# Optimization experiments

Measured on AMD Instinct MI355X. Metric: run time of the kernel, lower is better.

## Reference

```python
import jax, jax.numpy as jnp
import numpy as np

B, L, D, K = 1024, 50, 128, 20
NI, NL, NT = 100000, 10000, 2000  # items, locs, times


def _emb(k, n, d):
    e = jax.random.normal(k, (n, d), dtype=jnp.float32) * 0.02
    return e.at[0].set(0.0)  # padding_idx=0


def setup_inputs() -> dict:
    key = jax.random.key(0)
    ks = jax.random.split(key, 40)
    inp = {}
    inp['item'] = jax.random.randint(ks[0], (B, L), 0, NI)
    inp['locs'] = jax.random.randint(ks[1], (B,), 0, NL)
    inp['times'] = jax.random.randint(ks[2], (B,), 0, NT)
    inp['session_emb'] = jax.random.normal(ks[3], (B, 1, D), dtype=jnp.float32)
    # embedding tables
    inp['loc_emb'] = _emb(ks[4], NL, D)
    inp['time_emb'] = _emb(ks[5], NT, D)
    inp['item_emb'] = _emb(ks[6], NI, D)
    # sampled fixed-fanout neighbor tables Hg[edge]['neighbor']
    inp['nb_IL'] = jax.random.randint(ks[7], (NL, K), 0, NI)   # item neighbors of locs
    inp['nb_TL'] = jax.random.randint(ks[8], (NL, K), 0, NT)   # time neighbors of locs
    inp['nb_IT'] = jax.random.randint(ks[9], (NT, K), 0, NI)   # item neighbors of times
    inp['nb_LT'] = jax.random.randint(ks[10], (NT, K), 0, NL)  # loc neighbors of times
    inp['nb_II'] = jax.random.randint(ks[11], (NI, K), 0, NI)  # item neighbors of items
    inp['nb_LI'] = jax.random.randint(ks[12], (NI, K), 0, NL)  # loc neighbors of items
    inp['nb_TI'] = jax.random.randint(ks[13], (NI, K), 0, NT)  # time neighbors of items
    # 7 HeteAggregator params: Linear(2D -> D) + ReLU
    s = 1.0 / np.sqrt(2 * D)
    names = ['IL', 'TL', 'IT', 'LT', 'II', 'LI', 'TI']
    for i, nm in enumerate(names):
        inp['W_' + nm] = jax.random.uniform(ks[14 + i], (2 * D, D), jnp.float32, -s, s)
        inp['b_' + nm] = jnp.zeros((D,), jnp.float32)
    # 3 SemanticAttention params: Linear(D->D,bias)+tanh, Linear(D->1,no bias)
    s2 = 1.0 / np.sqrt(D)
    for i, nm in enumerate(['l', 't', 'i']):
        inp['Ws_' + nm] = jax.random.uniform(ks[24 + 3 * i], (D, D), jnp.float32, -s2, s2)
        inp['bs_' + nm] = jnp.zeros((D,), jnp.float32)
        inp['q_' + nm] = jax.random.uniform(ks[25 + 3 * i], (D, 1), jnp.float32, -s2, s2)
    return inp


def hete_agg(h_self, h_neigh, W, b):
    # h_self: [N, D]; h_neigh: [N, K, D] -> mean-aggregate, concat, linear, relu
    agg = h_neigh.mean(axis=1)
    return jax.nn.relu(jnp.concatenate([h_self, agg], axis=-1) @ W + b)


def sem_att(z, Ws, bs, q):
    # HAN-style semantic attention. z: [N, M, D]
    w = jnp.tanh(z @ Ws + bs) @ q          # [N, M, 1]
    beta = jax.nn.softmax(w.mean(axis=0), axis=0)  # [M, 1]
    return (beta[None] * z).sum(axis=1)    # [N, D]


def reference(item, locs, times, session_emb,
              loc_emb, time_emb, item_emb,
              nb_IL, nb_TL, nb_IT, nb_LT, nb_II, nb_LI, nb_TI,
              W_IL, b_IL, W_TL, b_TL, W_IT, b_IT, W_LT, b_LT,
              W_II, b_II, W_LI, b_LI, W_TI, b_TI,
              Ws_l, bs_l, q_l, Ws_t, bs_t, q_t, Ws_i, bs_i, q_i):
    iids = item.reshape(-1)  # [B*L]
    h_l_IL = hete_agg(loc_emb[locs], item_emb[nb_IL[locs]], W_IL, b_IL)
    h_l_TL = hete_agg(loc_emb[locs], time_emb[nb_TL[locs]], W_TL, b_TL)
    h_t_IT = hete_agg(time_emb[times], item_emb[nb_IT[times]], W_IT, b_IT)
    h_t_LT = hete_agg(time_emb[times], loc_emb[nb_LT[times]], W_LT, b_LT)
    h_i_II = hete_agg(item_emb[iids], item_emb[nb_II[iids]], W_II, b_II)
    h_i_LI = hete_agg(item_emb[iids], loc_emb[nb_LI[iids]], W_LI, b_LI)
    h_i_TI = hete_agg(item_emb[iids], time_emb[nb_TI[iids]], W_TI, b_TI)
    h_s = session_emb.squeeze(1)  # [B, D]
    h_l_stack = jnp.stack([h_l_IL, h_l_TL, h_s], axis=1)
    h_t_stack = jnp.stack([h_t_IT, h_t_LT, h_s], axis=1)
    h_i_stack = jnp.stack([h_i_II, h_i_TI, h_i_LI], axis=1)
    h_items = sem_att(h_i_stack, Ws_i, bs_i, q_i)
    h_locs = sem_att(h_l_stack, Ws_l, bs_l, q_l)
    h_times = sem_att(h_t_stack, Ws_t, bs_t, q_t)
    return (h_items, h_locs, h_times)
```

## Files before the change

kernel.cpp:

```cpp
#include <hip/hip_runtime.h>
#include <hip/hip_fp16.h>

#define DD 128
#define KK 20
#define TRR 32
#define NT 512

typedef unsigned int uint_t;
typedef unsigned short ushort_t;
typedef unsigned char uchar_t;
typedef _Float16 f16x8 __attribute__((ext_vector_type(8)));
typedef _Float16 f16x2 __attribute__((ext_vector_type(2)));
typedef float f32x4 __attribute__((ext_vector_type(4)));
typedef float f32x2 __attribute__((ext_vector_type(2)));

union UH { __half h; ushort_t s; };
union UF { f16x2 v[4]; uint4 u4; };

#if __has_builtin(__builtin_amdgcn_cvt_scalef32_pk_f16_fp8)
#define HAVE_SCALEF32 1
#endif

__device__ __forceinline__ float fast_tanh(float x) {
  const float e = __expf(2.f * x);
  return 1.f - 2.f / (e + 1.f);
}

__device__ __forceinline__ void f8acc(f16x2* a, const uint2 v) {
#ifdef HAVE_SCALEF32
  a[0] += __builtin_amdgcn_cvt_scalef32_pk_f16_fp8(v.x, 1.0f, false);
  a[1] += __builtin_amdgcn_cvt_scalef32_pk_f16_fp8(v.x, 1.0f, true);
  a[2] += __builtin_amdgcn_cvt_scalef32_pk_f16_fp8(v.y, 1.0f, false);
  a[3] += __builtin_amdgcn_cvt_scalef32_pk_f16_fp8(v.y, 1.0f, true);
#else
  f32x2 p;
  p = __builtin_amdgcn_cvt_pk_f32_fp8(v.x, false);
  a[0] += __builtin_amdgcn_cvt_pkrtz(p[0], p[1]);
  p = __builtin_amdgcn_cvt_pk_f32_fp8(v.x, true);
  a[1] += __builtin_amdgcn_cvt_pkrtz(p[0], p[1]);
  p = __builtin_amdgcn_cvt_pk_f32_fp8(v.y, false);
  a[2] += __builtin_amdgcn_cvt_pkrtz(p[0], p[1]);
  p = __builtin_amdgcn_cvt_pk_f32_fp8(v.y, true);
  a[3] += __builtin_amdgcn_cvt_pkrtz(p[0], p[1]);
#endif
}

struct CvtArgs {
  const float* item; const float* loc; const float* timet;
  ushort_t* dst16; uchar_t* dst8;
};

__global__ __launch_bounds__(256)
void k_cvt3(CvtArgs a) {
  const int t = blockIdx.x * blockDim.x + threadIdx.x;
  const float* src;
  if (t < 1600000) src = a.item + (size_t)t * 8;
  else if (t < 1760000) src = a.loc + ((size_t)t - 1600000) * 8;
  else src = a.timet + ((size_t)t - 1760000) * 8;
  const float4* ip = reinterpret_cast<const float4*>(src);
  const float4 x = ip[0], y = ip[1];
  UH h[8];
  h[0].h = __float2half_rn(x.x); h[1].h = __float2half_rn(x.y);
  h[2].h = __float2half_rn(x.z); h[3].h = __float2half_rn(x.w);
  h[4].h = __float2half_rn(y.x); h[5].h = __float2half_rn(y.y);
  h[6].h = __float2half_rn(y.z); h[7].h = __float2half_rn(y.w);
  uint4 o;
  o.x = (uint_t)h[0].s | ((uint_t)h[1].s << 16);
  o.y = (uint_t)h[2].s | ((uint_t)h[3].s << 16);
  o.z = (uint_t)h[4].s | ((uint_t)h[5].s << 16);
  o.w = (uint_t)h[6].s | ((uint_t)h[7].s << 16);
  reinterpret_cast<uint4*>(a.dst16)[t] = o;
  uint_t p0 = __builtin_amdgcn_cvt_pk_fp8_f32(x.x, x.y, 0u, false);
  p0 = __builtin_amdgcn_cvt_pk_fp8_f32(x.z, x.w, p0, true);
  uint_t p1 = __builtin_amdgcn_cvt_pk_fp8_f32(y.x, y.y, 0u, false);
  p1 = __builtin_amdgcn_cvt_pk_fp8_f32(y.z, y.w, p1, true);
  uint2 q; q.x = p0; q.y = p1;
  reinterpret_cast<uint2*>(a.dst8)[t] = q;
}

struct PackArgs {
  const float* src[10];
  ushort_t* dst;
};

__global__ __launch_bounds__(256)
void k_pack10(PackArgs a) {
  const int b = blockIdx.x, tid = threadIdx.x;
  int job, tin;
  size_t doff;
  if (b < 112) {
    job = b >> 4; tin = ((b & 15) << 8) | tid;
    doff = (size_t)job * 32768;
  } else {
    job = 7 + ((b - 112) >> 3); tin = (((b - 112) & 7) << 8) | tid;
    doff = 7ull * 32768 + (size_t)(job - 7) * 16384;
  }
  const float* W = a.src[job];
  const int l = tin & 63;
  const int ktnt = tin >> 6;
  const int nt = ktnt & 7;
  const int kt = ktnt >> 3;
  const int col = nt * 16 + (l & 15);
  const int kb = kt * 32 + ((l >> 4) << 3);
  UH h[8];
#pragma unroll
  for (int j = 0; j < 8; ++j) h[j].h = __float2half_rn(W[(size_t)(kb + j) * DD + col]);
  uint4 o;
  o.x = (uint_t)h[0].s | ((uint_t)h[1].s << 16);
  o.y = (uint_t)h[2].s | ((uint_t)h[3].s << 16);
  o.z = (uint_t)h[4].s | ((uint_t)h[5].s << 16);
  o.w = (uint_t)h[6].s | ((uint_t)h[7].s << 16);
  *reinterpret_cast<uint4*>(a.dst + doff + (size_t)ktnt * 512 + l * 8) = o;
}

struct MegaArgs {
  const int* item_idx; const ushort_t* item_t;
  const int* nbI[3]; const uchar_t* embI[3]; const ushort_t* pWI[3]; const float* bI[3];
  const ushort_t* pWsI; const float* bsI; const float* qI;
  ushort_t* hI; float* wsumI;
  const int* sidx[2]; const ushort_t* st[2];
  const int* nbS[2][2]; const uchar_t* embS[2][2];
  const ushort_t* pWS[2][2]; const float* bS[2][2];
  const ushort_t* pWsS[2]; const float* bsS[2]; const float* qS[2];
  const float* session;
  ushort_t* hS[2]; float* wsumS[2];
};

__global__ __launch_bounds__(NT, 6)
void k_mega(MegaArgs a) {
  __shared__ int ids[TRR];
  __shared__ int nidx[3][TRR][KK];
  __shared__ __align__(16) ushort_t xs[TRR][4 * DD + 8];
  __shared__ float red[8][TRR];

  const int tid = threadIdx.x;
  const int l = tid & 63;
  const int w = tid >> 6;
  const int bid = blockIdx.x;

  const bool isS = bid < 64;
  const int g = isS ? (bid >> 5) : 0;
  const int bl = isS ? (bid & 31) : (bid - 64);
  const int n0 = bl * TRR;

  const int* sidx;
  const ushort_t* selft;
  const int* nb_[3];
  const uchar_t* emb_[3];
  const ushort_t* pW_[3];
  const float* bias_[3];
  const ushort_t* pws; const float* bss; const float* qp;
  ushort_t* hd; float* wbase;
  if (!isS) {
    sidx = a.item_idx; selft = a.item_t;
    nb_[0] = a.nbI[0]; nb_[1] = a.nbI[1]; nb_[2] = a.nbI[2];
    emb_[0] = a.embI[0]; emb_[1] = a.embI[1]; emb_[2] = a.embI[2];
    pW_[0] = a.pWI[0]; pW_[1] = a.pWI[1]; pW_[2] = a.pWI[2];
    bias_[0] = a.bI[0]; bias_[1] = a.bI[1]; bias_[2] = a.bI[2];
    pws = a.pWsI; bss = a.bsI; qp = a.qI;
    hd = a.hI; wbase = a.wsumI;
  } else if (g == 0) {
    sidx = a.sidx[0]; selft = a.st[0];
    nb_[0] = a.nbS[0][0]; nb_[1] = a.nbS[0][1]; nb_[2] = nullptr;
    emb_[0] = a.embS[0][0]; emb_[1] = a.embS[0][1]; emb_[2] = nullptr;
    pW_[0] = a.pWS[0][0]; pW_[1] = a.pWS[0][1]; pW_[2] = nullptr;
    bias_[0] = a.bS[0][0]; bias_[1] = a.bS[0][1]; bias_[2] = nullptr;
    pws = a.pWsS[0]; bss = a.bsS[0]; qp = a.qS[0];
    hd = a.hS[0]; wbase = a.wsumS[0];
  } else {
    sidx = a.sidx[1]; selft = a.st[1];
    nb_[0] = a.nbS[1][0]; nb_[1] = a.nbS[1][1]; nb_[2] = nullptr;
    emb_[0] = a.embS[1][0]; emb_[1] = a.embS[1][1]; emb_[2] = nullptr;
    pW_[0] = a.pWS[1][0]; pW_[1] = a.pWS[1][1]; pW_[2] = nullptr;
    bias_[0] = a.bS[1][0]; bias_[1] = a.bS[1][1]; bias_[2] = nullptr;
    pws = a.pWsS[1]; bss = a.bsS[1]; qp = a.qS[1];
    hd = a.hS[1]; wbase = a.wsumS[1];
  }

  if (tid < TRR) ids[tid] = sidx[n0 + tid];
  __syncthreads();

  const int gr = tid >> 4;
  const int gsl = tid & 15;

#pragma unroll
  for (int e = 0; e < 3; ++e) {
    if (nb_[e]) {
      for (int t = tid; t < TRR * KK; t += NT) {
        const int rr = t / KK, kk = t - rr * KK;
        nidx[e][rr][kk] = nb_[e][(size_t)ids[rr] * KK + kk];
      }
    }
  }
  *reinterpret_cast<uint4*>(&xs[gr][gsl * 8]) =
      *reinterpret_cast<const uint4*>(selft + ((size_t)ids[gr] << 7) + gsl * 8);
  __syncthreads();

  const _Float16 sch = (_Float16)(1.f / KK);
  const f16x2 scv = (f16x2){sch, sch};
  if (!isS) {
    UF A0, A1, A2;
#pragma unroll
    for (int i = 0; i < 4; ++i) {
      A0.v[i] = (f16x2)0; A1.v[i] = (f16x2)0; A2.v[i] = (f16x2)0;
    }
#pragma unroll
    for (int kb = 0; kb < KK; kb += 4) {
      uint2 u0[4], u1[4], u2[4];
#pragma unroll
      for (int j = 0; j < 4; ++j)
        u0[j] = *reinterpret_cast<const uint2*>(emb_[0] + ((size_t)nidx[0][gr][kb + j] << 7) + gsl * 8);
#pragma unroll
      for (int j = 0; j < 4; ++j)
        u1[j] = *reinterpret_cast<const uint2*>(emb_[1] + ((size_t)nidx[1][gr][kb + j] << 7) + gsl * 8);
#pragma unroll
      for (int j = 0; j < 4; ++j)
        u2[j] = *reinterpret_cast<const uint2*>(emb_[2] + ((size_t)nidx[2][gr][kb + j] << 7) + gsl * 8);
#pragma unroll
      for (int j = 0; j < 4; ++j) {
        f8acc(A0.v, u0[j]); f8acc(A1.v, u1[j]); f8acc(A2.v, u2[j]);
      }
    }
#pragma unroll
    for (int i = 0; i < 4; ++i) {
      A0.v[i] *= scv; A1.v[i] *= scv; A2.v[i] *= scv;
    }
    *reinterpret_cast<uint4*>(&xs[gr][1 * DD + gsl * 8]) = A0.u4;
    *reinterpret_cast<uint4*>(&xs[gr][2 * DD + gsl * 8]) = A1.u4;
    *reinterpret_cast<uint4*>(&xs[gr][3 * DD + gsl * 8]) = A2.u4;
  } else {
    UF A0, A1;
#pragma unroll
    for (int i = 0; i < 4; ++i) { A0.v[i] = (f16x2)0; A1.v[i] = (f16x2)0; }
#pragma unroll
    for (int kb = 0; kb < KK; kb += 5) {
      uint2 u0[5], u1[5];
#pragma unroll
      for (int j = 0; j < 5; ++j)
        u0[j] = *reinterpret_cast<const uint2*>(emb_[0] + ((size_t)nidx[0][gr][kb + j] << 7) + gsl * 8);
#pragma unroll
      for (int j = 0; j < 5; ++j)
        u1[j] = *reinterpret_cast<const uint2*>(emb_[1] + ((size_t)nidx[1][gr][kb + j] << 7) + gsl * 8);
#pragma unroll
      for (int j = 0; j < 5; ++j) { f8acc(A0.v, u0[j]); f8acc(A1.v, u1[j]); }
    }
#pragma unroll
    for (int i = 0; i < 4; ++i) { A0.v[i] *= scv; A1.v[i] *= scv; }
    *reinterpret_cast<uint4*>(&xs[gr][1 * DD + gsl * 8]) = A0.u4;
    *reinterpret_cast<uint4*>(&xs[gr][2 * DD + gsl * 8]) = A1.u4;
    const float* srow = a.session + (size_t)(n0 + gr) * DD + gsl * 8;
    const float4 v0 = *reinterpret_cast<const float4*>(srow);
    const float4 v1 = *reinterpret_cast<const float4*>(srow + 4);
    UH h0, h1, h2, h3, h4, h5, h6, h7;
    h0.h = __float2half_rn(v0.x); h1.h = __float2half_rn(v0.y);
    h2.h = __float2half_rn(v0.z); h3.h = __float2half_rn(v0.w);
    h4.h = __float2half_rn(v1.x); h5.h = __float2half_rn(v1.y);
    h6.h = __float2half_rn(v1.z); h7.h = __float2half_rn(v1.w);
    uint4 o;
    o.x = (uint_t)h0.s | ((uint_t)h1.s << 16);
    o.y = (uint_t)h2.s | ((uint_t)h3.s << 16);
    o.z = (uint_t)h4.s | ((uint_t)h5.s << 16);
    o.w = (uint_t)h6.s | ((uint_t)h7.s << 16);
    *reinterpret_cast<uint4*>(&xs[gr][3 * DD + gsl * 8]) = o;
    *reinterpret_cast<uint4*>(hd + (size_t)(n0 + gr) * 3 * DD + 2 * DD + gsl * 8) = o;
  }
  __syncthreads();

  const int lcol = l & 15;
  const int g8 = (l >> 4) << 3;
  const int col0 = w * 16 + lcol;

#pragma unroll
  for (int e = 0; e < 3; ++e) {
    const bool full = (!isS) || (e < 2);
    if (full) {
      const ushort_t* pWp = pW_[e];
      const float* bp = bias_[e];
      f32x4 acc0, acc1;
      {
        const float b0 = bp[col0];
        acc0 = (f32x4){b0, b0, b0, b0};
        acc1 = acc0;
#pragma unroll
        for (int kt = 0; kt < 8; ++kt) {
          const int xcol = (kt < 4) ? (kt * 32 + g8) : (e * DD + kt * 32 + g8);
          const f16x8 Aa = *reinterpret_cast<const f16x8*>((const void*)&xs[lcol][xcol]);
          const f16x8 Ab = *reinterpret_cast<const f16x8*>((const void*)&xs[16 + lcol][xcol]);
          const f16x8 B = *reinterpret_cast<const f16x8*>(
              (const void*)(pWp + ((size_t)(kt * 8 + w) * 512) + l * 8));
          acc0 = __builtin_amdgcn_mfma_f32_16x16x32_f16(Aa, B, acc0, 0, 0, 0);
          acc1 = __builtin_amdgcn_mfma_f32_16x16x32_f16(Ab, B, acc1, 0, 0, 0);
        }
#pragma unroll
        for (int j = 0; j < 4; ++j) {
          acc0[j] = fmaxf(acc0[j], 0.f);
          acc1[j] = fmaxf(acc1[j], 0.f);
        }
      }
      __syncthreads();
      {
        const int rbase = (l >> 4) << 2;
#pragma unroll
        for (int j = 0; j < 4; ++j) {
          const int r0 = rbase + j, r1 = 16 + rbase + j;
          UH h0, h1;
          h0.h = __float2half_rn(acc0[j]);
          h1.h = __float2half_rn(acc1[j]);
          hd[(size_t)(n0 + r0) * 3 * DD + e * DD + col0] = h0.s;
          hd[(size_t)(n0 + r1) * 3 * DD + e * DD + col0] = h1.s;
          xs[r0][(e + 1) * DD + col0] = h0.s;
          xs[r1][(e + 1) * DD + col0] = h1.s;
        }
      }
      __syncthreads();
    }
    {
      const float b0 = bss[col0];
      f32x4 s0 = (f32x4){b0, b0, b0, b0};
      f32x4 s1 = s0;
#pragma unroll
      for (int kt = 0; kt < 4; ++kt) {
        const f16x8 Aa = *reinterpret_cast<const f16x8*>(
            (const void*)&xs[lcol][(e + 1) * DD + kt * 32 + g8]);
        const f16x8 Ab = *reinterpret_cast<const f16x8*>(
            (const void*)&xs[16 + lcol][(e + 1) * DD + kt * 32 + g8]);
        const f16x8 B = *reinterpret_cast<const f16x8*>(
            (const void*)(pws + ((size_t)(kt * 8 + w) * 512) + l * 8));
        s0 = __builtin_amdgcn_mfma_f32_16x16x32_f16(Aa, B, s0, 0, 0, 0);
        s1 = __builtin_amdgcn_mfma_f32_16x16x32_f16(Ab, B, s1, 0, 0, 0);
      }
      const float q0 = qp[col0];
      float p0[4], p1[4];
#pragma unroll
      for (int j = 0; j < 4; ++j) {
        p0[j] = fast_tanh(s0[j]) * q0;
        p1[j] = fast_tanh(s1[j]) * q0;
      }
#pragma unroll
      for (int off = 1; off < 16; off <<= 1) {
#pragma unroll
        for (int j = 0; j < 4; ++j) {
          p0[j] += __shfl_xor(p0[j], off, 64);
          p1[j] += __shfl_xor(p1[j], off, 64);
        }
      }
      if (lcol == 0) {
        const int rbase = (l >> 4) << 2;
#pragma unroll
        for (int j = 0; j < 4; ++j) {
          red[w][rbase + j] = p0[j];
          red[w][16 + rbase + j] = p1[j];
        }
      }
    }
    __syncthreads();
    if (tid < TRR) {
      float s = 0.f;
#pragma unroll
      for (int ww = 0; ww < 8; ++ww) s += red[ww][tid];
#pragma unroll
      for (int off = 1; off < 32; off <<= 1) s += __shfl_xor(s, off, 64);
      if (tid == 0) atomicAdd(&wbase[(bl & 63) * 4 + e], s);
    }
    __syncthreads();
  }
}

__global__ void k_beta(const float* __restrict__ wsum, float* __restrict__ beta) {
  if (threadIdx.x == 0 && blockIdx.x == 0) {
    const float invN[3] = {1.f / 51200.f, 1.f / 1024.f, 1.f / 1024.f};
    for (int g = 0; g < 3; ++g) {
      float s0 = 0.f, s1 = 0.f, s2 = 0.f;
      for (int bkt = 0; bkt < 64; ++bkt) {
        s0 += wsum[g * 256 + bkt * 4 + 0];
        s1 += wsum[g * 256 + bkt * 4 + 1];
        s2 += wsum[g * 256 + bkt * 4 + 2];
      }
      s0 *= invN[g]; s1 *= invN[g]; s2 *= invN[g];
      const float mx = fmaxf(s0, fmaxf(s1, s2));
      const float e0 = expf(s0 - mx), e1 = expf(s1 - mx), e2 = expf(s2 - mx);
      const float inv = 1.f / (e0 + e1 + e2);
      beta[g * 4 + 0] = e0 * inv;
      beta[g * 4 + 1] = e1 * inv;
      beta[g * 4 + 2] = e2 * inv;
    }
  }
}

__global__ void k_out(const ushort_t* __restrict__ h, const float* __restrict__ beta,
                      float* __restrict__ out) {
  const int idx = blockIdx.x * blockDim.x + threadIdx.x;
  const int row = idx >> 7;
  const int g = (row < 51200) ? 0 : ((row < 52224) ? 1 : 2);
  const float* bt = beta + g * 4;
  const size_t base = (size_t)idx + (size_t)row * 2 * DD;
  UH a, b, c;
  a.s = h[base]; b.s = h[base + DD]; c.s = h[base + 2 * DD];
  out[idx] = bt[0] * __half2float(a.h) + bt[1] * __half2float(b.h) +
             bt[2] * __half2float(c.h);
}


extern "C" void kernel_launch(void* const* d_in, const int* in_sizes, int n_in,
                              void* d_out, int out_size, void* d_ws, size_t ws_size,
                              hipStream_t stream) {
  const int*   item     = (const int*)  d_in[0];
  const int*   locs     = (const int*)  d_in[1];
  const int*   times    = (const int*)  d_in[2];
  const float* session  = (const float*)d_in[3];
  const float* loc_emb  = (const float*)d_in[4];
  const float* time_emb = (const float*)d_in[5];
  const float* item_emb = (const float*)d_in[6];
  const int* nb_IL = (const int*)d_in[7];
  const int* nb_TL = (const int*)d_in[8];
  const int* nb_IT = (const int*)d_in[9];
  const int* nb_LT = (const int*)d_in[10];
  const int* nb_II = (const int*)d_in[11];
  const int* nb_LI = (const int*)d_in[12];
  const int* nb_TI = (const int*)d_in[13];
  const float* W_IL = (const float*)d_in[14]; const float* b_IL = (const float*)d_in[15];
  const float* W_TL = (const float*)d_in[16]; const float* b_TL = (const float*)d_in[17];
  const float* W_IT = (const float*)d_in[18]; const float* b_IT = (const float*)d_in[19];
  const float* W_LT = (const float*)d_in[20]; const float* b_LT = (const float*)d_in[21];
  const float* W_II = (const float*)d_in[22]; const float* b_II = (const float*)d_in[23];
  const float* W_LI = (const float*)d_in[24]; const float* b_LI = (const float*)d_in[25];
  const float* W_TI = (const float*)d_in[26]; const float* b_TI = (const float*)d_in[27];
  const float* Ws_l = (const float*)d_in[28]; const float* bs_l = (const float*)d_in[29];
  const float* q_l  = (const float*)d_in[30];
  const float* Ws_t = (const float*)d_in[31]; const float* bs_t = (const float*)d_in[32];
  const float* q_t  = (const float*)d_in[33];
  const float* Ws_i = (const float*)d_in[34]; const float* bs_i = (const float*)d_in[35];
  const float* q_i  = (const float*)d_in[36];

  float* outp = (float*)d_out;

  char* wsb = (char*)d_ws;
  float* wsum  = (float*)wsb;
  float* betap = (float*)wsb + 1024;
  ushort_t* pk = (ushort_t*)(wsb + 16384);
  ushort_t* pk_II = pk;
  ushort_t* pk_TI = pk_II + 32768;
  ushort_t* pk_LI = pk_TI + 32768;
  ushort_t* pk_IL = pk_LI + 32768;
  ushort_t* pk_TL = pk_IL + 32768;
  ushort_t* pk_IT = pk_TL + 32768;
  ushort_t* pk_LT = pk_IT + 32768;
  ushort_t* pk_Wi = pk_LT + 32768;
  ushort_t* pk_Wl = pk_Wi + 16384;
  ushort_t* pk_Wt = pk_Wl + 16384;
  ushort_t* hbuf  = pk_Wt + 16384;
  ushort_t* item_h = hbuf + (size_t)53248 * 3 * DD;
  ushort_t* loc_h  = item_h + (size_t)100000 * DD;
  ushort_t* time_h = loc_h + (size_t)10000 * DD;
  uchar_t* item_8 = (uchar_t*)(time_h + (size_t)2000 * DD);
  uchar_t* loc_8  = item_8 + (size_t)100000 * DD;
  uchar_t* time_8 = loc_8 + (size_t)10000 * DD;

  hipMemsetAsync(d_ws, 0, 16384, stream);

  CvtArgs ca;
  ca.item = item_emb; ca.loc = loc_emb; ca.timet = time_emb;
  ca.dst16 = item_h; ca.dst8 = item_8;
  k_cvt3<<<dim3(7000), dim3(256), 0, stream>>>(ca);

  PackArgs pa;
  pa.src[0] = W_II; pa.src[1] = W_TI; pa.src[2] = W_LI;
  pa.src[3] = W_IL; pa.src[4] = W_TL; pa.src[5] = W_IT; pa.src[6] = W_LT;
  pa.src[7] = Ws_i; pa.src[8] = Ws_l; pa.src[9] = Ws_t;
  pa.dst = pk;
  k_pack10<<<dim3(136), dim3(256), 0, stream>>>(pa);

  ushort_t* h_items = hbuf;
  ushort_t* h_locs  = hbuf + (size_t)51200 * 3 * DD;
  ushort_t* h_times = hbuf + (size_t)52224 * 3 * DD;

  MegaArgs ma;
  ma.item_idx = item; ma.item_t = item_h;
  ma.nbI[0] = nb_II; ma.nbI[1] = nb_TI; ma.nbI[2] = nb_LI;
  ma.embI[0] = item_8; ma.embI[1] = time_8; ma.embI[2] = loc_8;
  ma.pWI[0] = pk_II; ma.pWI[1] = pk_TI; ma.pWI[2] = pk_LI;
  ma.bI[0] = b_II; ma.bI[1] = b_TI; ma.bI[2] = b_LI;
  ma.pWsI = pk_Wi; ma.bsI = bs_i; ma.qI = q_i;
  ma.hI = h_items; ma.wsumI = wsum + 0;
  ma.sidx[0] = locs;  ma.sidx[1] = times;
  ma.st[0] = loc_h;   ma.st[1] = time_h;
  ma.nbS[0][0] = nb_IL; ma.nbS[0][1] = nb_TL;
  ma.nbS[1][0] = nb_IT; ma.nbS[1][1] = nb_LT;
  ma.embS[0][0] = item_8; ma.embS[0][1] = time_8;
  ma.embS[1][0] = item_8; ma.embS[1][1] = loc_8;
  ma.pWS[0][0] = pk_IL; ma.pWS[0][1] = pk_TL;
  ma.pWS[1][0] = pk_IT; ma.pWS[1][1] = pk_LT;
  ma.bS[0][0] = b_IL; ma.bS[0][1] = b_TL;
  ma.bS[1][0] = b_IT; ma.bS[1][1] = b_LT;
  ma.pWsS[0] = pk_Wl; ma.pWsS[1] = pk_Wt;
  ma.bsS[0] = bs_l; ma.bsS[1] = bs_t;
  ma.qS[0] = q_l; ma.qS[1] = q_t;
  ma.session = session;
  ma.hS[0] = h_locs; ma.hS[1] = h_times;
  ma.wsumS[0] = wsum + 256; ma.wsumS[1] = wsum + 512;
  k_mega<<<dim3(64 + 51200 / TRR), dim3(NT), 0, stream>>>(ma);

  k_beta<<<dim3(1), dim3(64), 0, stream>>>(wsum, betap);
  k_out<<<dim3((53248 * 128) / 256), dim3(256), 0, stream>>>(hbuf, betap, outp);
}
```

Before: 123.0 us.

## Drop fp16 table copies, gather self rows from fp32, widen gathers and output stores

The conversion kernel no longer writes fp16 copies of all three embedding tables; the main kernel now reads self rows directly from the fp32 tables and converts them in registers. This removes a large write of about 28 MB of fp16 data per call. The item neighbour gather switches to 16-byte fp8 loads, but only half the threads (256) do the gathering, so fewer loads are in flight. The output kernel is vectorised to process four columns per thread with 8-byte loads and 16-byte stores.

```diff
diff --git a/kernel.cpp b/kernel.cpp
--- a/kernel.cpp
+++ b/kernel.cpp
@@ -11,11 +11,13 @@
 typedef unsigned char uchar_t;
 typedef _Float16 f16x8 __attribute__((ext_vector_type(8)));
 typedef _Float16 f16x2 __attribute__((ext_vector_type(2)));
+typedef __fp16 h16x2 __attribute__((ext_vector_type(2)));
 typedef float f32x4 __attribute__((ext_vector_type(4)));
 typedef float f32x2 __attribute__((ext_vector_type(2)));
 
 union UH { __half h; ushort_t s; };
 union UF { f16x2 v[4]; uint4 u4; };
+union CV { h16x2 a; f16x2 b; };
 
 #if __has_builtin(__builtin_amdgcn_cvt_scalef32_pk_f16_fp8)
 #define HAVE_SCALEF32 1
@@ -26,28 +28,57 @@
   return 1.f - 2.f / (e + 1.f);
 }
 
-__device__ __forceinline__ void f8acc(f16x2* a, const uint2 v) {
+__device__ __forceinline__ UF f8cvt(const uint2 v) {
+  UF r;
 #ifdef HAVE_SCALEF32
-  a[0] += __builtin_amdgcn_cvt_scalef32_pk_f16_fp8(v.x, 1.0f, false);
-  a[1] += __builtin_amdgcn_cvt_scalef32_pk_f16_fp8(v.x, 1.0f, true);
-  a[2] += __builtin_amdgcn_cvt_scalef32_pk_f16_fp8(v.y, 1.0f, false);
-  a[3] += __builtin_amdgcn_cvt_scalef32_pk_f16_fp8(v.y, 1.0f, true);
+  r.v[0] = __builtin_amdgcn_cvt_scalef32_pk_f16_fp8(v.x, 1.0f, false);
+  r.v[1] = __builtin_amdgcn_cvt_scalef32_pk_f16_fp8(v.x, 1.0f, true);
+  r.v[2] = __builtin_amdgcn_cvt_scalef32_pk_f16_fp8(v.y, 1.0f, false);
+  r.v[3] = __builtin_amdgcn_cvt_scalef32_pk_f16_fp8(v.y, 1.0f, true);
 #else
   f32x2 p;
+  CV c;
   p = __builtin_amdgcn_cvt_pk_f32_fp8(v.x, false);
-  a[0] += __builtin_amdgcn_cvt_pkrtz(p[0], p[1]);
+  c.a = __builtin_amdgcn_cvt_pkrtz(p[0], p[1]); r.v[0] = c.b;
   p = __builtin_amdgcn_cvt_pk_f32_fp8(v.x, true);
-  a[1] += __builtin_amdgcn_cvt_pkrtz(p[0], p[1]);
+  c.a = __builtin_amdgcn_cvt_pkrtz(p[0], p[1]); r.v[1] = c.b;
   p = __builtin_amdgcn_cvt_pk_f32_fp8(v.y, false);
-  a[2] += __builtin_amdgcn_cvt_pkrtz(p[0], p[1]);
+  c.a = __builtin_amdgcn_cvt_pkrtz(p[0], p[1]); r.v[2] = c.b;
   p = __builtin_amdgcn_cvt_pk_f32_fp8(v.y, true);
-  a[3] += __builtin_amdgcn_cvt_pkrtz(p[0], p[1]);
+  c.a = __builtin_amdgcn_cvt_pkrtz(p[0], p[1]); r.v[3] = c.b;
 #endif
+  return r;
+}
+
+__device__ __forceinline__ void f8acc(f16x2* a, const uint2 v) {
+  const UF r = f8cvt(v);
+  a[0] += r.v[0]; a[1] += r.v[1]; a[2] += r.v[2]; a[3] += r.v[3];
+}
+
+__device__ __forceinline__ void f8acc16(f16x2* a, const uint4 v) {
+  uint2 lo; lo.x = v.x; lo.y = v.y;
+  uint2 hi; hi.x = v.z; hi.y = v.w;
+  f8acc(a, lo);
+  f8acc(a + 4, hi);
+}
+
+__device__ __forceinline__ uint4 packf32x8(const float4 v0, const float4 v1) {
+  UH h0, h1, h2, h3, h4, h5, h6, h7;
+  h0.h = __float2half_rn(v0.x); h1.h = __float2half_rn(v0.y);
+  h2.h = __float2half_rn(v0.z); h3.h = __float2half_rn(v0.w);
+  h4.h = __float2half_rn(v1.x); h5.h = __float2half_rn(v1.y);
+  h6.h = __float2half_rn(v1.z); h7.h = __float2half_rn(v1.w);
+  uint4 o;
+  o.x = (uint_t)h0.s | ((uint_t)h1.s << 16);
+  o.y = (uint_t)h2.s | ((uint_t)h3.s << 16);
+  o.z = (uint_t)h4.s | ((uint_t)h5.s << 16);
+  o.w = (uint_t)h6.s | ((uint_t)h7.s << 16);
+  return o;
 }
 
 struct CvtArgs {
   const float* item; const float* loc; const float* timet;
-  ushort_t* dst16; uchar_t* dst8;
+  uchar_t* dst8;
 };
 
 __global__ __launch_bounds__(256)
@@ -59,17 +90,6 @@
   else src = a.timet + ((size_t)t - 1760000) * 8;
   const float4* ip = reinterpret_cast<const float4*>(src);
   const float4 x = ip[0], y = ip[1];
-  UH h[8];
-  h[0].h = __float2half_rn(x.x); h[1].h = __float2half_rn(x.y);
-  h[2].h = __float2half_rn(x.z); h[3].h = __float2half_rn(x.w);
-  h[4].h = __float2half_rn(y.x); h[5].h = __float2half_rn(y.y);
-  h[6].h = __float2half_rn(y.z); h[7].h = __float2half_rn(y.w);
-  uint4 o;
-  o.x = (uint_t)h[0].s | ((uint_t)h[1].s << 16);
-  o.y = (uint_t)h[2].s | ((uint_t)h[3].s << 16);
-  o.z = (uint_t)h[4].s | ((uint_t)h[5].s << 16);
-  o.w = (uint_t)h[6].s | ((uint_t)h[7].s << 16);
-  reinterpret_cast<uint4*>(a.dst16)[t] = o;
   uint_t p0 = __builtin_amdgcn_cvt_pk_fp8_f32(x.x, x.y, 0u, false);
   p0 = __builtin_amdgcn_cvt_pk_fp8_f32(x.z, x.w, p0, true);
   uint_t p1 = __builtin_amdgcn_cvt_pk_fp8_f32(y.x, y.y, 0u, false);
@@ -114,11 +134,11 @@
 }
 
 struct MegaArgs {
-  const int* item_idx; const ushort_t* item_t;
+  const int* item_idx; const float* item_f;
   const int* nbI[3]; const uchar_t* embI[3]; const ushort_t* pWI[3]; const float* bI[3];
   const ushort_t* pWsI; const float* bsI; const float* qI;
   ushort_t* hI; float* wsumI;
-  const int* sidx[2]; const ushort_t* st[2];
+  const int* sidx[2]; const float* st_f[2];
   const int* nbS[2][2]; const uchar_t* embS[2][2];
   const ushort_t* pWS[2][2]; const float* bS[2][2];
   const ushort_t* pWsS[2]; const float* bsS[2]; const float* qS[2];
@@ -144,7 +164,7 @@
   const int n0 = bl * TRR;
 
   const int* sidx;
-  const ushort_t* selft;
+  const float* selfF;
   const int* nb_[3];
   const uchar_t* emb_[3];
   const ushort_t* pW_[3];
@@ -152,7 +172,7 @@
   const ushort_t* pws; const float* bss; const float* qp;
   ushort_t* hd; float* wbase;
   if (!isS) {
-    sidx = a.item_idx; selft = a.item_t;
+    sidx = a.item_idx; selfF = a.item_f;
     nb_[0] = a.nbI[0]; nb_[1] = a.nbI[1]; nb_[2] = a.nbI[2];
     emb_[0] = a.embI[0]; emb_[1] = a.embI[1]; emb_[2] = a.embI[2];
     pW_[0] = a.pWI[0]; pW_[1] = a.pWI[1]; pW_[2] = a.pWI[2];
@@ -160,7 +180,7 @@
     pws = a.pWsI; bss = a.bsI; qp = a.qI;
     hd = a.hI; wbase = a.wsumI;
   } else if (g == 0) {
-    sidx = a.sidx[0]; selft = a.st[0];
+    sidx = a.sidx[0]; selfF = a.st_f[0];
     nb_[0] = a.nbS[0][0]; nb_[1] = a.nbS[0][1]; nb_[2] = nullptr;
     emb_[0] = a.embS[0][0]; emb_[1] = a.embS[0][1]; emb_[2] = nullptr;
     pW_[0] = a.pWS[0][0]; pW_[1] = a.pWS[0][1]; pW_[2] = nullptr;
@@ -168,7 +188,7 @@
     pws = a.pWsS[0]; bss = a.bsS[0]; qp = a.qS[0];
     hd = a.hS[0]; wbase = a.wsumS[0];
   } else {
-    sidx = a.sidx[1]; selft = a.st[1];
+    sidx = a.sidx[1]; selfF = a.st_f[1];
     nb_[0] = a.nbS[1][0]; nb_[1] = a.nbS[1][1]; nb_[2] = nullptr;
     emb_[0] = a.embS[1][0]; emb_[1] = a.embS[1][1]; emb_[2] = nullptr;
     pW_[0] = a.pWS[1][0]; pW_[1] = a.pWS[1][1]; pW_[2] = nullptr;
@@ -192,42 +212,63 @@
       }
     }
   }
-  *reinterpret_cast<uint4*>(&xs[gr][gsl * 8]) =
-      *reinterpret_cast<const uint4*>(selft + ((size_t)ids[gr] << 7) + gsl * 8);
+  {
+    const float* sp = selfF + ((size_t)ids[gr] << 7) + gsl * 8;
+    const float4 v0 = *reinterpret_cast<const float4*>(sp);
+    const float4 v1 = *reinterpret_cast<const float4*>(sp + 4);
+    *reinterpret_cast<uint4*>(&xs[gr][gsl * 8]) = packf32x8(v0, v1);
+  }
   __syncthreads();
 
   const _Float16 sch = (_Float16)(1.f / KK);
   const f16x2 scv = (f16x2){sch, sch};
+  const int lcol = l & 15;
+  const int g8 = (l >> 4) << 3;
+  const int col0 = w * 16 + lcol;
+
   if (!isS) {
-    UF A0, A1, A2;
-#pragma unroll
-    for (int i = 0; i < 4; ++i) {
-      A0.v[i] = (f16x2)0; A1.v[i] = (f16x2)0; A2.v[i] = (f16x2)0;
-    }
-#pragma unroll
-    for (int kb = 0; kb < KK; kb += 4) {
-      uint2 u0[4], u1[4], u2[4];
-#pragma unroll
-      for (int j = 0; j < 4; ++j)
-        u0[j] = *reinterpret_cast<const uint2*>(emb_[0] + ((size_t)nidx[0][gr][kb + j] << 7) + gsl * 8);
-#pragma unroll
-      for (int j = 0; j < 4; ++j)
-        u1[j] = *reinterpret_cast<const uint2*>(emb_[1] + ((size_t)nidx[1][gr][kb + j] << 7) + gsl * 8);
-#pragma unroll
-      for (int j = 0; j < 4; ++j)
-        u2[j] = *reinterpret_cast<const uint2*>(emb_[2] + ((size_t)nidx[2][gr][kb + j] << 7) + gsl * 8);
-#pragma unroll
-      for (int j = 0; j < 4; ++j) {
-        f8acc(A0.v, u0[j]); f8acc(A1.v, u1[j]); f8acc(A2.v, u2[j]);
-      }
-    }
-#pragma unroll
-    for (int i = 0; i < 4; ++i) {
-      A0.v[i] *= scv; A1.v[i] *= scv; A2.v[i] *= scv;
-    }
-    *reinterpret_cast<uint4*>(&xs[gr][1 * DD + gsl * 8]) = A0.u4;
-    *reinterpret_cast<uint4*>(&xs[gr][2 * DD + gsl * 8]) = A1.u4;
-    *reinterpret_cast<uint4*>(&xs[gr][3 * DD + gsl * 8]) = A2.u4;
+    if (tid < 256) {
+      const int r = tid >> 3;
+      const int sl = tid & 7;
+      f16x2 a0[8], a1[8], a2[8];
+#pragma unroll
+      for (int i = 0; i < 8; ++i) { a0[i] = (f16x2)0; a1[i] = (f16x2)0; a2[i] = (f16x2)0; }
+#pragma unroll
+      for (int kb = 0; kb < KK; kb += 2) {
+        uint4 u0[2], u1[2], u2[2];
+#pragma unroll
+        for (int j = 0; j < 2; ++j)
+          u0[j] = *reinterpret_cast<const uint4*>(
+              emb_[0] + ((size_t)nidx[0][r][kb + j] << 7) + sl * 16);
+#pragma unroll
+        for (int j = 0; j < 2; ++j)
+          u1[j] = *reinterpret_cast<const uint4*>(
+              emb_[1] + ((size_t)nidx[1][r][kb + j] << 7) + sl * 16);
+#pragma unroll
+        for (int j = 0; j < 2; ++j)
+          u2[j] = *reinterpret_cast<const uint4*>(
+              emb_[2] + ((size_t)nidx[2][r][kb + j] << 7) + sl * 16);
+#pragma unroll
+        for (int j = 0; j < 2; ++j) {
+          f8acc16(a0, u0[j]); f8acc16(a1, u1[j]); f8acc16(a2, u2[j]);
+        }
+      }
+#pragma unroll
+      for (int i = 0; i < 8; ++i) { a0[i] *= scv; a1[i] *= scv; a2[i] *= scv; }
+      UF P;
+      P.v[0] = a0[0]; P.v[1] = a0[1]; P.v[2] = a0[2]; P.v[3] = a0[3];
+      *reinterpret_cast<uint4*>(&xs[r][1 * DD + sl * 16]) = P.u4;
+      P.v[0] = a0[4]; P.v[1] = a0[5]; P.v[2] = a0[6]; P.v[3] = a0[7];
+      *reinterpret_cast<uint4*>(&xs[r][1 * DD + sl * 16 + 8]) = P.u4;
+      P.v[0] = a1[0]; P.v[1] = a1[1]; P.v[2] = a1[2]; P.v[3] = a1[3];
+      *reinterpret_cast<uint4*>(&xs[r][2 * DD + sl * 16]) = P.u4;
+      P.v[0] = a1[4]; P.v[1] = a1[5]; P.v[2] = a1[6]; P.v[3] = a1[7];
+      *reinterpret_cast<uint4*>(&xs[r][2 * DD + sl * 16 + 8]) = P.u4;
+      P.v[0] = a2[0]; P.v[1] = a2[1]; P.v[2] = a2[2]; P.v[3] = a2[3];
+      *reinterpret_cast<uint4*>(&xs[r][3 * DD + sl * 16]) = P.u4;
+      P.v[0] = a2[4]; P.v[1] = a2[5]; P.v[2] = a2[6]; P.v[3] = a2[7];
+      *reinterpret_cast<uint4*>(&xs[r][3 * DD + sl * 16 + 8]) = P.u4;
+    }
   } else {
     UF A0, A1;
 #pragma unroll
@@ -237,10 +278,12 @@
       uint2 u0[5], u1[5];
 #pragma unroll
       for (int j = 0; j < 5; ++j)
-        u0[j] = *reinterpret_cast<const uint2*>(emb_[0] + ((size_t)nidx[0][gr][kb + j] << 7) + gsl * 8);
+        u0[j] = *reinterpret_cast<const uint2*>(
+            emb_[0] + ((size_t)nidx[0][gr][kb + j] << 7) + gsl * 8);
 #pragma unroll
       for (int j = 0; j < 5; ++j)
-        u1[j] = *reinterpret_cast<const uint2*>(emb_[1] + ((size_t)nidx[1][gr][kb + j] << 7) + gsl * 8);
+        u1[j] = *reinterpret_cast<const uint2*>(
+            emb_[1] + ((size_t)nidx[1][gr][kb + j] << 7) + gsl * 8);
 #pragma unroll
       for (int j = 0; j < 5; ++j) { f8acc(A0.v, u0[j]); f8acc(A1.v, u1[j]); }
     }
@@ -251,24 +294,11 @@
     const float* srow = a.session + (size_t)(n0 + gr) * DD + gsl * 8;
     const float4 v0 = *reinterpret_cast<const float4*>(srow);
     const float4 v1 = *reinterpret_cast<const float4*>(srow + 4);
-    UH h0, h1, h2, h3, h4, h5, h6, h7;
-    h0.h = __float2half_rn(v0.x); h1.h = __float2half_rn(v0.y);
-    h2.h = __float2half_rn(v0.z); h3.h = __float2half_rn(v0.w);
-    h4.h = __float2half_rn(v1.x); h5.h = __float2half_rn(v1.y);
-    h6.h = __float2half_rn(v1.z); h7.h = __float2half_rn(v1.w);
-    uint4 o;
-    o.x = (uint_t)h0.s | ((uint_t)h1.s << 16);
-    o.y = (uint_t)h2.s | ((uint_t)h3.s << 16);
-    o.z = (uint_t)h4.s | ((uint_t)h5.s << 16);
-    o.w = (uint_t)h6.s | ((uint_t)h7.s << 16);
+    const uint4 o = packf32x8(v0, v1);
     *reinterpret_cast<uint4*>(&xs[gr][3 * DD + gsl * 8]) = o;
     *reinterpret_cast<uint4*>(hd + (size_t)(n0 + gr) * 3 * DD + 2 * DD + gsl * 8) = o;
   }
   __syncthreads();
-
-  const int lcol = l & 15;
-  const int g8 = (l >> 4) << 3;
-  const int col0 = w * 16 + lcol;
 
 #pragma unroll
   for (int e = 0; e < 3; ++e) {
@@ -387,17 +417,34 @@
   }
 }
 
-__global__ void k_out(const ushort_t* __restrict__ h, const float* __restrict__ beta,
-                      float* __restrict__ out) {
-  const int idx = blockIdx.x * blockDim.x + threadIdx.x;
-  const int row = idx >> 7;
+__global__ __launch_bounds__(256)
+void k_out(const ushort_t* __restrict__ h, const float* __restrict__ beta,
+           float* __restrict__ out) {
+  const int t = blockIdx.x * blockDim.x + threadIdx.x;
+  const int row = t >> 5;
+  const int c0 = (t & 31) * 4;
   const int g = (row < 51200) ? 0 : ((row < 52224) ? 1 : 2);
   const float* bt = beta + g * 4;
-  const size_t base = (size_t)idx + (size_t)row * 2 * DD;
-  UH a, b, c;
-  a.s = h[base]; b.s = h[base + DD]; c.s = h[base + 2 * DD];
-  out[idx] = bt[0] * __half2float(a.h) + bt[1] * __half2float(b.h) +
-             bt[2] * __half2float(c.h);
+  const size_t base = (size_t)row * 3 * DD + c0;
+  const ushort4 ha = *reinterpret_cast<const ushort4*>(&h[base]);
+  const ushort4 hb = *reinterpret_cast<const ushort4*>(&h[base + DD]);
+  const ushort4 hc = *reinterpret_cast<const ushort4*>(&h[base + 2 * DD]);
+  UH u;
+  float4 o;
+  float va, vb, vc;
+  u.s = ha.x; va = __half2float(u.h); u.s = hb.x; vb = __half2float(u.h);
+  u.s = hc.x; vc = __half2float(u.h);
+  o.x = bt[0] * va + bt[1] * vb + bt[2] * vc;
+  u.s = ha.y; va = __half2float(u.h); u.s = hb.y; vb = __half2float(u.h);
+  u.s = hc.y; vc = __half2float(u.h);
+  o.y = bt[0] * va + bt[1] * vb + bt[2] * vc;
+  u.s = ha.z; va = __half2float(u.h); u.s = hb.z; vb = __half2float(u.h);
+  u.s = hc.z; vc = __half2float(u.h);
+  o.z = bt[0] * va + bt[1] * vb + bt[2] * vc;
+  u.s = ha.w; va = __half2float(u.h); u.s = hb.w; vb = __half2float(u.h);
+  u.s = hc.w; vc = __half2float(u.h);
+  o.w = bt[0] * va + bt[1] * vb + bt[2] * vc;
+  *reinterpret_cast<float4*>(&out[(size_t)row * DD + c0]) = o;
 }
 
 
@@ -449,18 +496,15 @@
   ushort_t* pk_Wl = pk_Wi + 16384;
   ushort_t* pk_Wt = pk_Wl + 16384;
   ushort_t* hbuf  = pk_Wt + 16384;
-  ushort_t* item_h = hbuf + (size_t)53248 * 3 * DD;
-  ushort_t* loc_h  = item_h + (size_t)100000 * DD;
-  ushort_t* time_h = loc_h + (size_t)10000 * DD;
-  uchar_t* item_8 = (uchar_t*)(time_h + (size_t)2000 * DD);
+  uchar_t* item_8 = (uchar_t*)(hbuf + (size_t)53248 * 3 * DD);
   uchar_t* loc_8  = item_8 + (size_t)100000 * DD;
   uchar_t* time_8 = loc_8 + (size_t)10000 * DD;
 
-  hipMemsetAsync(d_ws, 0, 16384, stream);
+  (void)hipMemsetAsync(d_ws, 0, 16384, stream);
 
   CvtArgs ca;
   ca.item = item_emb; ca.loc = loc_emb; ca.timet = time_emb;
-  ca.dst16 = item_h; ca.dst8 = item_8;
+  ca.dst8 = item_8;
   k_cvt3<<<dim3(7000), dim3(256), 0, stream>>>(ca);
 
   PackArgs pa;
@@ -475,7 +519,7 @@
   ushort_t* h_times = hbuf + (size_t)52224 * 3 * DD;
 
   MegaArgs ma;
-  ma.item_idx = item; ma.item_t = item_h;
+  ma.item_idx = item; ma.item_f = item_emb;
   ma.nbI[0] = nb_II; ma.nbI[1] = nb_TI; ma.nbI[2] = nb_LI;
   ma.embI[0] = item_8; ma.embI[1] = time_8; ma.embI[2] = loc_8;
   ma.pWI[0] = pk_II; ma.pWI[1] = pk_TI; ma.pWI[2] = pk_LI;
@@ -483,7 +527,7 @@
   ma.pWsI = pk_Wi; ma.bsI = bs_i; ma.qI = q_i;
   ma.hI = h_items; ma.wsumI = wsum + 0;
   ma.sidx[0] = locs;  ma.sidx[1] = times;
-  ma.st[0] = loc_h;   ma.st[1] = time_h;
+  ma.st_f[0] = loc_emb; ma.st_f[1] = time_emb;
   ma.nbS[0][0] = nb_IL; ma.nbS[0][1] = nb_TL;
   ma.nbS[1][0] = nb_IT; ma.nbS[1][1] = nb_LT;
   ma.embS[0][0] = item_8; ma.embS[0][1] = time_8;
@@ -501,5 +545,5 @@
   k_mega<<<dim3(64 + 51200 / TRR), dim3(NT), 0, stream>>>(ma);
 
   k_beta<<<dim3(1), dim3(64), 0, stream>>>(wsum, betap);
-  k_out<<<dim3((53248 * 128) / 256), dim3(256), 0, stream>>>(hbuf, betap, outp);
-}
+  k_out<<<dim3((53248 * 32) / 256), dim3(256), 0, stream>>>(hbuf, betap, outp);
+}
```

Measured after the change: 118.2 us. -3.9%, faster.
